# Kernel optimization log

Hardware: AMD Instinct MI355X
Metric: run time of the kernel (lower is better)

The kernel has to match this reference:

```python
import jax, jax.numpy as jnp
import numpy as np

B, S, D_IN, D_MODEL, H = 2, 2048, 1024, 1024, 16
DEPTH = D_MODEL // H


def setup_inputs() -> dict:
    key = jax.random.key(0)
    ks = jax.random.split(key, 12)
    f32 = jnp.float32
    scale = 0.02  # typical init scale for linear weights
    inp = {
        "v": jax.random.normal(ks[0], (B, S, D_IN), f32),
        "k": jax.random.normal(ks[1], (B, S, D_IN), f32),
        "q": jax.random.normal(ks[2], (B, S, D_IN), f32),
        # padding mask: 1 -> masked out, 0 -> keep; broadcastable to (B,H,Sq,Sk)
        "mask": jax.random.randint(ks[3], (B, 1, 1, S), 0, 2).astype(f32),
        # linear params stored as [in, out] so y = x @ W + b (matches torch Linear math)
        "Wq": jax.random.normal(ks[4], (D_IN, D_MODEL), f32) * scale,
        "bq": jnp.zeros((D_MODEL,), f32),
        "Wk": jax.random.normal(ks[5], (D_IN, D_MODEL), f32) * scale,
        "bk": jnp.zeros((D_MODEL,), f32),
        "Wv": jax.random.normal(ks[6], (D_IN, D_MODEL), f32) * scale,
        "bv": jnp.zeros((D_MODEL,), f32),
        "Wo": jax.random.normal(ks[7], (D_MODEL, D_MODEL), f32) * scale,
        "bo": jnp.zeros((D_MODEL,), f32),
    }
    return inp


def _split_heads(x):
    # [B, S, D_MODEL] -> [B, H, S, DEPTH]
    b = x.shape[0]
    return x.reshape(b, -1, H, DEPTH).transpose(0, 2, 1, 3)


def reference(v, k, q, mask, Wq, bq, Wk, bk, Wv, bv, Wo, bo):
    qh = _split_heads(q @ Wq + bq)   # [B,H,Sq,D]
    kh = _split_heads(k @ Wk + bk)   # [B,H,Sk,D]
    vh = _split_heads(v @ Wv + bv)   # [B,H,Sk,D]

    # scaled dot-product attention with additive mask (mask * -1e9)
    inv_sqrt_dk = 1.0 / jnp.sqrt(jnp.float32(DEPTH))
    logits = jnp.einsum('bhqd,bhkd->bhqk', qh, kh) * inv_sqrt_dk
    logits = logits + mask * (-1e9)
    attn = jax.nn.softmax(logits, axis=-1)          # [B,H,Sq,Sk]
    ctx = jnp.einsum('bhqk,bhkd->bhqd', attn, vh)   # [B,H,Sq,D]

    b = q.shape[0]
    concat = ctx.transpose(0, 2, 1, 3).reshape(b, -1, D_MODEL)  # [B,Sq,D_MODEL]
    out = concat @ Wo + bo
    return out, attn
```

## Files before the change

kernel.cpp:

```cpp
#include <hip/hip_runtime.h>
#include <cstdint>
#include <cstddef>

typedef __attribute__((ext_vector_type(4))) float f4;
typedef __attribute__((ext_vector_type(8))) short bf16x8;
typedef __attribute__((ext_vector_type(8))) unsigned short u16x8;
typedef unsigned long long u64;

__device__ __forceinline__ unsigned short f2bf(float x) {
    unsigned u = __float_as_uint(x);
    u += 0x7fffu + ((u >> 16) & 1u);
    return (unsigned short)(u >> 16);
}
__device__ __forceinline__ float bf2f(unsigned short h) {
    return __uint_as_float(((unsigned)h) << 16);
}
__device__ __forceinline__ float fast_exp2(float x) { return __builtin_amdgcn_exp2f(x); }
__device__ __forceinline__ float fast_log2(float x) { return __builtin_amdgcn_logf(x); }
__device__ __forceinline__ void gll16(const void* g, void* l) {
    __builtin_amdgcn_global_load_lds(
        (const __attribute__((address_space(1))) unsigned int*)g,
        (__attribute__((address_space(3))) unsigned int*)l, 16, 0, 0);
}
__device__ __forceinline__ f4 mfma16(bf16x8 a, bf16x8 b, f4 c) {
    return __builtin_amdgcn_mfma_f32_16x16x32_bf16(a, b, c, 0, 0, 0);
}

__global__ __launch_bounds__(256)
void prep_w_kernel(const float* __restrict__ Wq, const float* __restrict__ Wk,
                   const float* __restrict__ Wv, const float* __restrict__ Wo,
                   unsigned short* __restrict__ wt)
{
    const int w = blockIdx.z;
    const float* W = w == 0 ? Wq : (w == 1 ? Wk : (w == 2 ? Wv : Wo));
    unsigned short* hi = wt + (size_t)w * 1048576;

    const int kb = blockIdx.x << 6, nb = blockIdx.y << 6;
    __shared__ float T[64][68];
    const int tid = threadIdx.x;
    {
        const int r = tid >> 2, c0 = (tid & 3) << 4;
        const float* src = W + (size_t)(kb + r) * 1024 + nb + c0;
        *(f4*)&T[r][c0 + 0]  = *(const f4*)(src + 0);
        *(f4*)&T[r][c0 + 4]  = *(const f4*)(src + 4);
        *(f4*)&T[r][c0 + 8]  = *(const f4*)(src + 8);
        *(f4*)&T[r][c0 + 12] = *(const f4*)(src + 12);
    }
    __syncthreads();
    {
        const int n = tid & 63, ks = (tid >> 6) << 4;
        unsigned short vh[16];
        #pragma unroll
        for (int j = 0; j < 16; ++j) vh[j] = f2bf(T[ks + j][n]);
        const size_t dst = (size_t)(nb + n) * 1024 + kb + ks;
        *(u16x8*)(hi + dst)     = *(u16x8*)&vh[0];
        *(u16x8*)(hi + dst + 8) = *(u16x8*)&vh[8];
    }
}

__global__ __launch_bounds__(256)
void prep_a_kernel(const float* __restrict__ q, const float* __restrict__ k,
                   const float* __restrict__ v, unsigned short* __restrict__ a_hi)
{
    const int gid = blockIdx.x * 256 + threadIdx.x;
    const int z = gid >> 18;
    const int rem = gid & 262143;
    const float* src = z == 0 ? q : (z == 1 ? k : v);
    const size_t off = (size_t)rem << 4;
    const float* s = src + off;
    unsigned short* hi = a_hi + ((size_t)z << 22) + off;
    float xs[16];
    *(f4*)&xs[0]  = *(const f4*)(s + 0);
    *(f4*)&xs[4]  = *(const f4*)(s + 4);
    *(f4*)&xs[8]  = *(const f4*)(s + 8);
    *(f4*)&xs[12] = *(const f4*)(s + 12);
    unsigned short hv[16];
    #pragma unroll
    for (int j = 0; j < 16; ++j) hv[j] = f2bf(xs[j]);
    *(u16x8*)(hi + 0) = *(u16x8*)&hv[0];
    *(u16x8*)(hi + 8) = *(u16x8*)&hv[8];
}

__device__ __forceinline__ void gemm1_core(
    const unsigned short* __restrict__ AH, const unsigned short* __restrict__ WH,
    const float* __restrict__ bias, int bm, int bn, int mode,
    unsigned short* __restrict__ o_hi, float* __restrict__ o_f32, unsigned char* lds)
{
    unsigned char* As = lds;
    unsigned char* Bs = lds + 16384;

    const int tid = threadIdx.x, lane = tid & 63, wave = tid >> 6;
    const int wm = wave >> 1, wn = wave & 1;
    const int cx = lane & 15, lg = lane >> 4;
    const int l3 = lane >> 3, p3 = lane & 7;
    const int m0 = bm << 7, n0 = bn << 7;

    f4 acc[4][4];
    #pragma unroll
    for (int i = 0; i < 4; ++i)
        #pragma unroll
        for (int j = 0; j < 4; ++j) acc[i][j] = (f4){0.f, 0.f, 0.f, 0.f};

    #pragma unroll 1
    for (int k0 = 0; k0 < 1024; k0 += 64) {
        __syncthreads();
        #pragma unroll
        for (int c = 0; c < 4; ++c) {
            const int cb = (c << 2) + wave;
            const int row = (cb << 3) + l3;
            const int lgx = p3 ^ (row & 7);
            gll16(AH + (size_t)(m0 + row) * 1024 + k0 + (lgx << 3),
                  As + (cb << 10) + (lane << 4));
            gll16(WH + (size_t)(n0 + row) * 1024 + k0 + (lgx << 3),
                  Bs + (cb << 10) + (lane << 4));
        }
        __syncthreads();
        #pragma unroll
        for (int ks = 0; ks < 2; ++ks) {
            bf16x8 ah[4], bh[4];
            #pragma unroll
            for (int t = 0; t < 4; ++t) {
                const int r = (wm << 6) + (t << 4) + cx;
                ah[t] = *(const bf16x8*)(As + r * 128 + (((((ks << 2) + lg)) ^ (r & 7)) << 4));
                const int n = (wn << 6) + (t << 4) + cx;
                bh[t] = *(const bf16x8*)(Bs + n * 128 + (((((ks << 2) + lg)) ^ (n & 7)) << 4));
            }
            #pragma unroll
            for (int i = 0; i < 4; ++i)
                #pragma unroll
                for (int j = 0; j < 4; ++j)
                    acc[i][j] = mfma16(ah[i], bh[j], acc[i][j]);
        }
    }

    float bv4[4];
    #pragma unroll
    for (int j = 0; j < 4; ++j) bv4[j] = bias[n0 + (wn << 6) + (j << 4) + cx];

    #pragma unroll
    for (int i = 0; i < 4; ++i)
        #pragma unroll
        for (int j = 0; j < 4; ++j) {
            const int n = n0 + (wn << 6) + (j << 4) + cx;
            const int mb = m0 + (wm << 6) + (i << 4) + (lg << 2);
            if (mode == 2) {
                #pragma unroll
                for (int r = 0; r < 4; ++r)
                    o_f32[(size_t)(mb + r) * 1024 + n] = acc[i][j][r] + bv4[j];
            } else if (mode == 1) {
                const int b = mb >> 11, hh = n >> 6, d = n & 63;
                #pragma unroll
                for (int r = 0; r < 4; ++r) {
                    const int s = (mb + r) & 2047;
                    o_hi[(((size_t)(b * 16 + hh)) * 2048 + s) * 64 + d] = f2bf(acc[i][j][r] + bv4[j]);
                }
            } else {
                const int b = mb >> 11, s = mb & 2047;
                const int hh = n >> 6, d = n & 63;
                const unsigned short p0 = f2bf(acc[i][j][0] + bv4[j]);
                const unsigned short p1 = f2bf(acc[i][j][1] + bv4[j]);
                const unsigned short p2 = f2bf(acc[i][j][2] + bv4[j]);
                const unsigned short p3v = f2bf(acc[i][j][3] + bv4[j]);
                const u64 pk = (u64)p0 | ((u64)p1 << 16) | ((u64)p2 << 32) | ((u64)p3v << 48);
                *(u64*)&o_hi[((((size_t)(b * 16 + hh)) * 64 + d) << 11) + s] = pk;
            }
        }
}

__global__ __launch_bounds__(256)
void qkv_gemm_kernel(const unsigned short* __restrict__ a_hi,
                     const unsigned short* __restrict__ wt,
                     const float* __restrict__ bq, const float* __restrict__ bk,
                     const float* __restrict__ bv,
                     unsigned short* __restrict__ q_hi, unsigned short* __restrict__ k_hi,
                     unsigned short* __restrict__ vT)
{
    __shared__ __align__(16) unsigned char lds[32768];
    const int f = blockIdx.x;
    const int id2 = (f & 7) * 96 + (f >> 3);
    const int z = id2 >> 8;
    const int rem = id2 & 255;
    const int bn = rem >> 5, bm = rem & 31;
    const unsigned short* AH = a_hi + ((size_t)z << 22);
    const unsigned short* WH = wt + (size_t)z * 1048576;
    const float* bias = z == 0 ? bq : (z == 1 ? bk : bv);
    unsigned short* ohi = z == 0 ? q_hi : (z == 1 ? k_hi : vT);
    gemm1_core(AH, WH, bias, bm, bn, (z == 2) ? 3 : 1, ohi, nullptr, lds);
}

__global__ __launch_bounds__(256)
void out_gemm_kernel(const unsigned short* __restrict__ ctx_hi,
                     const unsigned short* __restrict__ wt_o,
                     const float* __restrict__ bo, float* __restrict__ out)
{
    __shared__ __align__(16) unsigned char lds[32768];
    const int f = blockIdx.x;
    const int id2 = (f & 7) * 32 + (f >> 3);
    const int bn = id2 >> 5, bm = id2 & 31;
    gemm1_core(ctx_hi, wt_o, bo, bm, bn, 2, nullptr, out, lds);
}

__global__ __launch_bounds__(256, 4)
void attn_kernel(const unsigned short* __restrict__ q_hi, const unsigned short* __restrict__ k_hi,
                 const unsigned short* __restrict__ vT, const float* __restrict__ mask,
                 float* __restrict__ attn, unsigned short* __restrict__ ctx_hi)
{
    __shared__ __align__(16) unsigned char lds[40960];
    unsigned char* K1 = lds;
    unsigned char* Vs = lds + 16384;
    unsigned char* Ps = lds + 32768;

    const int f = blockIdx.x;
    const int swzf = (f & 7) * 128 + (f >> 3);
    const int bh = swzf >> 5;
    const int q0 = (swzf & 31) << 6;
    const int b = bh >> 4, h = bh & 15;
    const int tid = threadIdx.x, lane = tid & 63, wave = tid >> 6;
    const int cx = lane & 15, lg = lane >> 4;
    const int l3 = lane >> 3, p3 = lane & 7;
    const size_t base = (size_t)bh * 131072;
    const float* mg = mask + (size_t)b * 2048;

    constexpr float C2   = 0.18033688011112042f;
    constexpr float M2   = -1.4426950408889634e9f;
    constexpr float MFIX = 4.0f;

    #pragma unroll
    for (int c = 0; c < 2; ++c) {
        const int cb = (c << 2) + wave;
        const int row = (cb << 3) + l3;
        const int lgx = p3 ^ (row & 7);
        gll16(q_hi + base + (size_t)(q0 + row) * 64 + (lgx << 3),
              Ps + (cb << 10) + (lane << 4));
        gll16(k_hi + base + (size_t)row * 64 + (lgx << 3),
              K1 + (cb << 10) + (lane << 4));
    }
    f4 mrc[4];
    #pragma unroll
    for (int nt = 0; nt < 4; ++nt) mrc[nt] = *(const f4*)(mg + (nt << 4) + (lg << 2));
    asm volatile("s_waitcnt vmcnt(0)" ::: "memory");
    __builtin_amdgcn_s_barrier();

    bf16x8 qb[2];
    {
        const int r = (wave << 4) + cx;
        const int mk = r & 7;
        #pragma unroll
        for (int ks = 0; ks < 2; ++ks)
            qb[ks] = *(const bf16x8*)(Ps + r * 128 + (((((ks << 2) + lg)) ^ mk) << 4));
    }

    float l_loc = 0.f;
    #pragma unroll 1
    for (int t = 0; t < 32; ++t) {
        const int p = t & 1;
        const int k0 = t << 6;
        f4 mrn[4];
        if (t < 31) {
            #pragma unroll
            for (int c = 0; c < 2; ++c) {
                const int cb = (c << 2) + wave;
                const int row = (cb << 3) + l3;
                const int lgx = p3 ^ (row & 7);
                gll16(k_hi + base + (size_t)(k0 + 64 + row) * 64 + (lgx << 3),
                      K1 + ((p ^ 1) << 13) + (cb << 10) + (lane << 4));
            }
            #pragma unroll
            for (int nt = 0; nt < 4; ++nt)
                mrn[nt] = *(const f4*)(mg + k0 + 64 + (nt << 4) + (lg << 2));
        }
        const unsigned char* Kc = K1 + (p << 13);
        #pragma unroll
        for (int nt = 0; nt < 4; ++nt) {
            const int kr = (nt << 4) + cx;
            const int mk = kr & 7;
            f4 s = (f4){0.f, 0.f, 0.f, 0.f};
            #pragma unroll
            for (int ks = 0; ks < 2; ++ks) {
                const bf16x8 kb = *(const bf16x8*)(Kc + kr * 128 + (((((ks << 2) + lg)) ^ mk) << 4));
                s = mfma16(kb, qb[ks], s);
            }
            #pragma unroll
            for (int r = 0; r < 4; ++r)
                l_loc += fast_exp2(fmaf(s[r], C2, fmaf(mrc[nt][r], M2, -MFIX)));
        }
        #pragma unroll
        for (int nt = 0; nt < 4; ++nt) mrc[nt] = mrn[nt];
        asm volatile("s_waitcnt vmcnt(4)" ::: "memory");
        __builtin_amdgcn_s_barrier();
    }
    float ssum = l_loc;
    ssum += __shfl_xor(ssum, 16);
    ssum += __shfl_xor(ssum, 32);
    const float cofs = -MFIX - fast_log2(ssum);

    #pragma unroll
    for (int c = 0; c < 2; ++c) {
        const int cb = (c << 2) + wave;
        const int row = (cb << 3) + l3;
        const int lgx = p3 ^ (row & 7);
        gll16(k_hi + base + (size_t)row * 64 + (lgx << 3),
              K1 + (cb << 10) + (lane << 4));
        gll16(vT + base + ((size_t)row << 11) + (lgx << 3),
              Vs + (cb << 10) + (lane << 4));
    }
    #pragma unroll
    for (int nt = 0; nt < 4; ++nt) mrc[nt] = *(const f4*)(mg + (nt << 4) + (lg << 2));
    asm volatile("s_waitcnt vmcnt(0)" ::: "memory");
    __builtin_amdgcn_s_barrier();

    f4 cacc[4];
    #pragma unroll
    for (int nt = 0; nt < 4; ++nt) cacc[nt] = (f4){0.f, 0.f, 0.f, 0.f};

    float* arow = attn + ((size_t)bh * 2048 + q0 + (wave << 4) + cx) * 2048;
    const unsigned psSwz = (unsigned)((cx & 7) << 4);

    #pragma unroll 1
    for (int t = 0; t < 32; ++t) {
        const int p = t & 1;
        const int k0 = t << 6;
        f4 mrn[4];
        if (t < 31) {
            #pragma unroll
            for (int c = 0; c < 2; ++c) {
                const int cb = (c << 2) + wave;
                const int row = (cb << 3) + l3;
                const int lgx = p3 ^ (row & 7);
                gll16(k_hi + base + (size_t)(k0 + 64 + row) * 64 + (lgx << 3),
                      K1 + ((p ^ 1) << 13) + (cb << 10) + (lane << 4));
                gll16(vT + base + ((size_t)row << 11) + k0 + 64 + (lgx << 3),
                      Vs + ((p ^ 1) << 13) + (cb << 10) + (lane << 4));
            }
            #pragma unroll
            for (int nt = 0; nt < 4; ++nt)
                mrn[nt] = *(const f4*)(mg + k0 + 64 + (nt << 4) + (lg << 2));
        }
        const unsigned char* Kc = K1 + (p << 13);
        f4 s[4];
        #pragma unroll
        for (int nt = 0; nt < 4; ++nt) {
            const int kr = (nt << 4) + cx;
            const int mk = kr & 7;
            s[nt] = (f4){0.f, 0.f, 0.f, 0.f};
            #pragma unroll
            for (int ks = 0; ks < 2; ++ks) {
                const bf16x8 kb = *(const bf16x8*)(Kc + kr * 128 + (((((ks << 2) + lg)) ^ mk) << 4));
                s[nt] = mfma16(kb, qb[ks], s[nt]);
            }
        }
        #pragma unroll
        for (int nt = 0; nt < 4; ++nt) {
            f4 pv;
            #pragma unroll
            for (int r = 0; r < 4; ++r)
                pv[r] = fast_exp2(fmaf(s[nt][r], C2, fmaf(mrc[nt][r], M2, cofs)));
            *(f4*)(arow + k0 + (nt << 4) + (lg << 2)) = pv;
            const unsigned w0 = (unsigned)f2bf(pv[0]) | ((unsigned)f2bf(pv[1]) << 16);
            const unsigned w1 = (unsigned)f2bf(pv[2]) | ((unsigned)f2bf(pv[3]) << 16);
            const u64 packed = (u64)w0 | ((u64)w1 << 32);
            *(u64*)(Ps + (((wave << 4) + cx) * 128) +
                    ((unsigned)((nt << 5) + (lg << 3)) ^ psSwz)) = packed;
        }
        #pragma unroll
        for (int nt = 0; nt < 4; ++nt) mrc[nt] = mrn[nt];
        #pragma unroll
        for (int ks = 0; ks < 2; ++ks) {
            const bf16x8 pa = *(const bf16x8*)(Ps + (((wave << 4) + cx) * 128) +
                                ((unsigned)((ks << 6) + (lg << 4)) ^ psSwz));
            #pragma unroll
            for (int nt = 0; nt < 4; ++nt) {
                const int dr = (nt << 4) + cx;
                const bf16x8 vb = *(const bf16x8*)(Vs + (p << 13) + dr * 128 +
                                    (((((ks << 2) + lg)) ^ (dr & 7)) << 4));
                cacc[nt] = mfma16(pa, vb, cacc[nt]);
            }
        }
        asm volatile("s_waitcnt vmcnt(8)" ::: "memory");
        __builtin_amdgcn_s_barrier();
    }

    #pragma unroll
    for (int nt = 0; nt < 4; ++nt)
        #pragma unroll
        for (int r = 0; r < 4; ++r) {
            const int srow = q0 + (wave << 4) + (lg << 2) + r;
            const int d = (h << 6) + (nt << 4) + cx;
            ctx_hi[((size_t)b * 2048 + srow) * 1024 + d] = f2bf(cacc[nt][r]);
        }
}

extern "C" void kernel_launch(void* const* d_in, const int* in_sizes, int n_in,
                              void* d_out, int out_size, void* d_ws, size_t ws_size,
                              hipStream_t stream)
{
    const float* v_in = (const float*)d_in[0];
    const float* k_in = (const float*)d_in[1];
    const float* q_in = (const float*)d_in[2];
    const float* mask = (const float*)d_in[3];
    const float* Wq = (const float*)d_in[4];
    const float* bq = (const float*)d_in[5];
    const float* Wk = (const float*)d_in[6];
    const float* bk = (const float*)d_in[7];
    const float* Wv = (const float*)d_in[8];
    const float* bv = (const float*)d_in[9];
    const float* Wo = (const float*)d_in[10];
    const float* bo = (const float*)d_in[11];

    float* out  = (float*)d_out;
    float* attn = out + (size_t)4194304;

    unsigned char* ws = (unsigned char*)d_ws;
    unsigned short* wt     = (unsigned short*)(ws);
    unsigned short* q_hi   = (unsigned short*)(ws + (size_t)(8)  * 1048576);
    unsigned short* k_hi   = (unsigned short*)(ws + (size_t)(16) * 1048576);
    unsigned short* vT     = (unsigned short*)(ws + (size_t)(24) * 1048576);
    unsigned short* ctx_hi = (unsigned short*)(ws + (size_t)(32) * 1048576);

    unsigned short* a_hi   = (unsigned short*)(attn + (size_t)60 * 1048576);

    prep_w_kernel<<<dim3(16, 16, 4), 256, 0, stream>>>(Wq, Wk, Wv, Wo, wt);
    prep_a_kernel<<<3072, 256, 0, stream>>>(q_in, k_in, v_in, a_hi);
    qkv_gemm_kernel<<<768, 256, 0, stream>>>(a_hi, wt, bq, bk, bv, q_hi, k_hi, vT);
    attn_kernel<<<1024, 256, 0, stream>>>(q_hi, k_hi, vT, mask, attn, ctx_hi);
    out_gemm_kernel<<<256, 256, 0, stream>>>(ctx_hi, wt + (size_t)3 * 1048576, bo, out);
}
```

Measured before the change: 308.3 us.

## Add separate V transpose kernel, set MFMA priority, retune attention waitcnts

The QKV GEMM now writes V in head-major [B,H,S,D] layout like Q and K, and a new LDS-based transpose kernel produces the transposed V used by attention. This replaces the scattered 8-byte transposed stores in the GEMM epilogue. The attention kernel wraps its MFMA sections in s_setprio to favour matrix issue, splits score computation from the exp accumulation, and changes the vmcnt wait thresholds, making the first pass wait on all loads. The cost is an extra kernel launch, an extra round trip of V through memory, and possibly less load overlap from the stricter waits.

```diff
diff --git a/kernel.cpp b/kernel.cpp
--- a/kernel.cpp
+++ b/kernel.cpp
@@ -81,6 +81,34 @@
     *(u16x8*)(hi + 8) = *(u16x8*)&hv[8];
 }
 
+__global__ __launch_bounds__(256)
+void vtr_kernel(const unsigned short* __restrict__ v_hi, unsigned short* __restrict__ vT)
+{
+    __shared__ unsigned short T[64][80];
+    const int bh = blockIdx.y;
+    const int s0 = blockIdx.x << 6;
+    const int tid = threadIdx.x;
+    const size_t base = (size_t)bh * 131072;
+    {
+        const int s = tid >> 2, dq = (tid & 3) << 4;
+        const unsigned short* src = v_hi + base + (size_t)(s0 + s) * 64 + dq;
+        u16x8 a = *(const u16x8*)src;
+        u16x8 b = *(const u16x8*)(src + 8);
+        *(u16x8*)&T[s][dq]     = a;
+        *(u16x8*)&T[s][dq + 8] = b;
+    }
+    __syncthreads();
+    {
+        const int d = tid >> 2, sq = (tid & 3) << 4;
+        unsigned short o[16];
+        #pragma unroll
+        for (int j = 0; j < 16; ++j) o[j] = T[sq + j][d];
+        unsigned short* dst = vT + base + ((size_t)d << 11) + s0 + sq;
+        *(u16x8*)dst       = *(u16x8*)&o[0];
+        *(u16x8*)(dst + 8) = *(u16x8*)&o[8];
+    }
+}
+
 __device__ __forceinline__ void gemm1_core(
     const unsigned short* __restrict__ AH, const unsigned short* __restrict__ WH,
     const float* __restrict__ bias, int bm, int bn, int mode,
@@ -147,22 +175,13 @@
                 #pragma unroll
                 for (int r = 0; r < 4; ++r)
                     o_f32[(size_t)(mb + r) * 1024 + n] = acc[i][j][r] + bv4[j];
-            } else if (mode == 1) {
+            } else {
                 const int b = mb >> 11, hh = n >> 6, d = n & 63;
                 #pragma unroll
                 for (int r = 0; r < 4; ++r) {
                     const int s = (mb + r) & 2047;
                     o_hi[(((size_t)(b * 16 + hh)) * 2048 + s) * 64 + d] = f2bf(acc[i][j][r] + bv4[j]);
                 }
-            } else {
-                const int b = mb >> 11, s = mb & 2047;
-                const int hh = n >> 6, d = n & 63;
-                const unsigned short p0 = f2bf(acc[i][j][0] + bv4[j]);
-                const unsigned short p1 = f2bf(acc[i][j][1] + bv4[j]);
-                const unsigned short p2 = f2bf(acc[i][j][2] + bv4[j]);
-                const unsigned short p3v = f2bf(acc[i][j][3] + bv4[j]);
-                const u64 pk = (u64)p0 | ((u64)p1 << 16) | ((u64)p2 << 32) | ((u64)p3v << 48);
-                *(u64*)&o_hi[((((size_t)(b * 16 + hh)) * 64 + d) << 11) + s] = pk;
             }
         }
 }
@@ -173,7 +192,7 @@
                      const float* __restrict__ bq, const float* __restrict__ bk,
                      const float* __restrict__ bv,
                      unsigned short* __restrict__ q_hi, unsigned short* __restrict__ k_hi,
-                     unsigned short* __restrict__ vT)
+                     unsigned short* __restrict__ v_hi)
 {
     __shared__ __align__(16) unsigned char lds[32768];
     const int f = blockIdx.x;
@@ -184,8 +203,8 @@
     const unsigned short* AH = a_hi + ((size_t)z << 22);
     const unsigned short* WH = wt + (size_t)z * 1048576;
     const float* bias = z == 0 ? bq : (z == 1 ? bk : bv);
-    unsigned short* ohi = z == 0 ? q_hi : (z == 1 ? k_hi : vT);
-    gemm1_core(AH, WH, bias, bm, bn, (z == 2) ? 3 : 1, ohi, nullptr, lds);
+    unsigned short* ohi = z == 0 ? q_hi : (z == 1 ? k_hi : v_hi);
+    gemm1_core(AH, WH, bias, bm, bn, 1, ohi, nullptr, lds);
 }
 
 __global__ __launch_bounds__(256)
@@ -270,6 +289,8 @@
                 mrn[nt] = *(const f4*)(mg + k0 + 64 + (nt << 4) + (lg << 2));
         }
         const unsigned char* Kc = K1 + (p << 13);
+        __builtin_amdgcn_s_setprio(1);
+        f4 sv[4];
         #pragma unroll
         for (int nt = 0; nt < 4; ++nt) {
             const int kr = (nt << 4) + cx;
@@ -280,13 +301,17 @@
                 const bf16x8 kb = *(const bf16x8*)(Kc + kr * 128 + (((((ks << 2) + lg)) ^ mk) << 4));
                 s = mfma16(kb, qb[ks], s);
             }
+            sv[nt] = s;
+        }
+        __builtin_amdgcn_s_setprio(0);
+        #pragma unroll
+        for (int nt = 0; nt < 4; ++nt)
             #pragma unroll
             for (int r = 0; r < 4; ++r)
-                l_loc += fast_exp2(fmaf(s[r], C2, fmaf(mrc[nt][r], M2, -MFIX)));
-        }
+                l_loc += fast_exp2(fmaf(sv[nt][r], C2, fmaf(mrc[nt][r], M2, -MFIX)));
         #pragma unroll
         for (int nt = 0; nt < 4; ++nt) mrc[nt] = mrn[nt];
-        asm volatile("s_waitcnt vmcnt(4)" ::: "memory");
+        asm volatile("s_waitcnt vmcnt(0)" ::: "memory");
         __builtin_amdgcn_s_barrier();
     }
     float ssum = l_loc;
@@ -338,6 +363,7 @@
         }
         const unsigned char* Kc = K1 + (p << 13);
         f4 s[4];
+        __builtin_amdgcn_s_setprio(1);
         #pragma unroll
         for (int nt = 0; nt < 4; ++nt) {
             const int kr = (nt << 4) + cx;
@@ -349,6 +375,7 @@
                 s[nt] = mfma16(kb, qb[ks], s[nt]);
             }
         }
+        __builtin_amdgcn_s_setprio(0);
         #pragma unroll
         for (int nt = 0; nt < 4; ++nt) {
             f4 pv;
@@ -364,6 +391,7 @@
         }
         #pragma unroll
         for (int nt = 0; nt < 4; ++nt) mrc[nt] = mrn[nt];
+        __builtin_amdgcn_s_setprio(1);
         #pragma unroll
         for (int ks = 0; ks < 2; ++ks) {
             const bf16x8 pa = *(const bf16x8*)(Ps + (((wave << 4) + cx) * 128) +
@@ -376,7 +404,8 @@
                 cacc[nt] = mfma16(pa, vb, cacc[nt]);
             }
         }
-        asm volatile("s_waitcnt vmcnt(8)" ::: "memory");
+        __builtin_amdgcn_s_setprio(0);
+        asm volatile("s_waitcnt vmcnt(4)" ::: "memory");
         __builtin_amdgcn_s_barrier();
     }
 
@@ -414,14 +443,16 @@
     unsigned short* wt     = (unsigned short*)(ws);
     unsigned short* q_hi   = (unsigned short*)(ws + (size_t)(8)  * 1048576);
     unsigned short* k_hi   = (unsigned short*)(ws + (size_t)(16) * 1048576);
-    unsigned short* vT     = (unsigned short*)(ws + (size_t)(24) * 1048576);
+    unsigned short* v_hi   = (unsigned short*)(ws + (size_t)(24) * 1048576);
     unsigned short* ctx_hi = (unsigned short*)(ws + (size_t)(32) * 1048576);
+    unsigned short* vT     = (unsigned short*)(ws + (size_t)(40) * 1048576);
 
     unsigned short* a_hi   = (unsigned short*)(attn + (size_t)60 * 1048576);
 
     prep_w_kernel<<<dim3(16, 16, 4), 256, 0, stream>>>(Wq, Wk, Wv, Wo, wt);
     prep_a_kernel<<<3072, 256, 0, stream>>>(q_in, k_in, v_in, a_hi);
-    qkv_gemm_kernel<<<768, 256, 0, stream>>>(a_hi, wt, bq, bk, bv, q_hi, k_hi, vT);
+    qkv_gemm_kernel<<<768, 256, 0, stream>>>(a_hi, wt, bq, bk, bv, q_hi, k_hi, v_hi);
+    vtr_kernel<<<dim3(32, 32), 256, 0, stream>>>(v_hi, vT);
     attn_kernel<<<1024, 256, 0, stream>>>(q_hi, k_hi, vT, mask, attn, ctx_hi);
     out_gemm_kernel<<<256, 256, 0, stream>>>(ctx_hi, wt + (size_t)3 * 1048576, bo, out);
 }
```

After: 293.2 us. 4.9% less time.

## Transpose V through LDS, prioritise MFMA waves, and pack bf16 conversions

Applied to the files above, without the earlier changes.

Adds a GEMM epilogue (mode 3) that stages the V projection tile in swizzled LDS and writes V^T with 16-byte vector stores, replacing scattered 8-byte transposed stores. In the attention kernel it raises wave priority around the MFMA blocks and adds scheduling barriers after the prefetch issue. It also splits the row-sum accumulator into four independent chains and uses the hardware packed bf16 conversion instruction for P. The vmcnt wait in the second loop is tightened from 8 to 4, which may add stall time. The old mode-0 epilogue is folded into the mode-1 path, so correctness depends on the launcher now passing mode 3 for V.

```diff
diff --git a/kernel.cpp b/kernel.cpp
--- a/kernel.cpp
+++ b/kernel.cpp
@@ -14,6 +14,11 @@
 }
 __device__ __forceinline__ float bf2f(unsigned short h) {
     return __uint_as_float(((unsigned)h) << 16);
+}
+__device__ __forceinline__ unsigned cvtpk_bf16(float lo, float hi) {
+    unsigned r;
+    asm("v_cvt_pk_bf16_f32 %0, %1, %2" : "=v"(r) : "v"(lo), "v"(hi));
+    return r;
 }
 __device__ __forceinline__ float fast_exp2(float x) { return __builtin_amdgcn_exp2f(x); }
 __device__ __forceinline__ float fast_log2(float x) { return __builtin_amdgcn_logf(x); }
@@ -137,6 +142,35 @@
     #pragma unroll
     for (int j = 0; j < 4; ++j) bv4[j] = bias[n0 + (wn << 6) + (j << 4) + cx];
 
+    if (mode == 3) {
+        __syncthreads();
+        unsigned short* T = (unsigned short*)lds;
+        #pragma unroll
+        for (int i = 0; i < 4; ++i)
+            #pragma unroll
+            for (int j = 0; j < 4; ++j) {
+                const int dl = (wn << 6) + (j << 4) + cx;
+                #pragma unroll
+                for (int r = 0; r < 4; ++r) {
+                    const int sl = (wm << 6) + (i << 4) + (lg << 2) + r;
+                    T[sl * 128 + (dl ^ ((sl & 7) << 3))] = f2bf(acc[i][j][r] + bv4[j]);
+                }
+            }
+        __syncthreads();
+        const int b = m0 >> 11, s0g = m0 & 2047;
+        const int dl = tid >> 1, sc = (tid & 1) << 6;
+        const int hh = (n0 + dl) >> 6, d = (n0 + dl) & 63;
+        unsigned short ov[64];
+        #pragma unroll
+        for (int j = 0; j < 64; ++j)
+            ov[j] = T[(sc + j) * 128 + (dl ^ (((sc + j) & 7) << 3))];
+        unsigned short* dst = o_hi + ((((size_t)(b * 16 + hh)) * 64 + d) << 11) + s0g + sc;
+        #pragma unroll
+        for (int c8 = 0; c8 < 8; ++c8)
+            *(u16x8*)(dst + (c8 << 3)) = *(u16x8*)&ov[c8 << 3];
+        return;
+    }
+
     #pragma unroll
     for (int i = 0; i < 4; ++i)
         #pragma unroll
@@ -147,22 +181,13 @@
                 #pragma unroll
                 for (int r = 0; r < 4; ++r)
                     o_f32[(size_t)(mb + r) * 1024 + n] = acc[i][j][r] + bv4[j];
-            } else if (mode == 1) {
+            } else {
                 const int b = mb >> 11, hh = n >> 6, d = n & 63;
                 #pragma unroll
                 for (int r = 0; r < 4; ++r) {
                     const int s = (mb + r) & 2047;
                     o_hi[(((size_t)(b * 16 + hh)) * 2048 + s) * 64 + d] = f2bf(acc[i][j][r] + bv4[j]);
                 }
-            } else {
-                const int b = mb >> 11, s = mb & 2047;
-                const int hh = n >> 6, d = n & 63;
-                const unsigned short p0 = f2bf(acc[i][j][0] + bv4[j]);
-                const unsigned short p1 = f2bf(acc[i][j][1] + bv4[j]);
-                const unsigned short p2 = f2bf(acc[i][j][2] + bv4[j]);
-                const unsigned short p3v = f2bf(acc[i][j][3] + bv4[j]);
-                const u64 pk = (u64)p0 | ((u64)p1 << 16) | ((u64)p2 << 32) | ((u64)p3v << 48);
-                *(u64*)&o_hi[((((size_t)(b * 16 + hh)) * 64 + d) << 11) + s] = pk;
             }
         }
 }
@@ -250,7 +275,7 @@
             qb[ks] = *(const bf16x8*)(Ps + r * 128 + (((((ks << 2) + lg)) ^ mk) << 4));
     }
 
-    float l_loc = 0.f;
+    float l4[4] = {0.f, 0.f, 0.f, 0.f};
     #pragma unroll 1
     for (int t = 0; t < 32; ++t) {
         const int p = t & 1;
@@ -265,11 +290,14 @@
                 gll16(k_hi + base + (size_t)(k0 + 64 + row) * 64 + (lgx << 3),
                       K1 + ((p ^ 1) << 13) + (cb << 10) + (lane << 4));
             }
+            __builtin_amdgcn_sched_barrier(0);
             #pragma unroll
             for (int nt = 0; nt < 4; ++nt)
                 mrn[nt] = *(const f4*)(mg + k0 + 64 + (nt << 4) + (lg << 2));
         }
         const unsigned char* Kc = K1 + (p << 13);
+        __builtin_amdgcn_s_setprio(1);
+        f4 sv[4];
         #pragma unroll
         for (int nt = 0; nt < 4; ++nt) {
             const int kr = (nt << 4) + cx;
@@ -280,16 +308,20 @@
                 const bf16x8 kb = *(const bf16x8*)(Kc + kr * 128 + (((((ks << 2) + lg)) ^ mk) << 4));
                 s = mfma16(kb, qb[ks], s);
             }
+            sv[nt] = s;
+        }
+        __builtin_amdgcn_s_setprio(0);
+        #pragma unroll
+        for (int nt = 0; nt < 4; ++nt)
             #pragma unroll
             for (int r = 0; r < 4; ++r)
-                l_loc += fast_exp2(fmaf(s[r], C2, fmaf(mrc[nt][r], M2, -MFIX)));
-        }
+                l4[nt] += fast_exp2(fmaf(sv[nt][r], C2, fmaf(mrc[nt][r], M2, -MFIX)));
         #pragma unroll
         for (int nt = 0; nt < 4; ++nt) mrc[nt] = mrn[nt];
         asm volatile("s_waitcnt vmcnt(4)" ::: "memory");
         __builtin_amdgcn_s_barrier();
     }
-    float ssum = l_loc;
+    float ssum = (l4[0] + l4[1]) + (l4[2] + l4[3]);
     ssum += __shfl_xor(ssum, 16);
     ssum += __shfl_xor(ssum, 32);
     const float cofs = -MFIX - fast_log2(ssum);
@@ -332,12 +364,14 @@
                 gll16(vT + base + ((size_t)row << 11) + k0 + 64 + (lgx << 3),
                       Vs + ((p ^ 1) << 13) + (cb << 10) + (lane << 4));
             }
+            __builtin_amdgcn_sched_barrier(0);
             #pragma unroll
             for (int nt = 0; nt < 4; ++nt)
                 mrn[nt] = *(const f4*)(mg + k0 + 64 + (nt << 4) + (lg << 2));
         }
         const unsigned char* Kc = K1 + (p << 13);
         f4 s[4];
+        __builtin_amdgcn_s_setprio(1);
         #pragma unroll
         for (int nt = 0; nt < 4; ++nt) {
             const int kr = (nt << 4) + cx;
@@ -349,6 +383,7 @@
                 s[nt] = mfma16(kb, qb[ks], s[nt]);
             }
         }
+        __builtin_amdgcn_s_setprio(0);
         #pragma unroll
         for (int nt = 0; nt < 4; ++nt) {
             f4 pv;
@@ -356,14 +391,15 @@
             for (int r = 0; r < 4; ++r)
                 pv[r] = fast_exp2(fmaf(s[nt][r], C2, fmaf(mrc[nt][r], M2, cofs)));
             *(f4*)(arow + k0 + (nt << 4) + (lg << 2)) = pv;
-            const unsigned w0 = (unsigned)f2bf(pv[0]) | ((unsigned)f2bf(pv[1]) << 16);
-            const unsigned w1 = (unsigned)f2bf(pv[2]) | ((unsigned)f2bf(pv[3]) << 16);
+            const unsigned w0 = cvtpk_bf16(pv[0], pv[1]);
+            const unsigned w1 = cvtpk_bf16(pv[2], pv[3]);
             const u64 packed = (u64)w0 | ((u64)w1 << 32);
             *(u64*)(Ps + (((wave << 4) + cx) * 128) +
                     ((unsigned)((nt << 5) + (lg << 3)) ^ psSwz)) = packed;
         }
         #pragma unroll
         for (int nt = 0; nt < 4; ++nt) mrc[nt] = mrn[nt];
+        __builtin_amdgcn_s_setprio(1);
         #pragma unroll
         for (int ks = 0; ks < 2; ++ks) {
             const bf16x8 pa = *(const bf16x8*)(Ps + (((wave << 4) + cx) * 128) +
@@ -376,7 +412,8 @@
                 cacc[nt] = mfma16(pa, vb, cacc[nt]);
             }
         }
-        asm volatile("s_waitcnt vmcnt(8)" ::: "memory");
+        __builtin_amdgcn_s_setprio(0);
+        asm volatile("s_waitcnt vmcnt(4)" ::: "memory");
         __builtin_amdgcn_s_barrier();
     }
 
```

Result: faster. 292.7 us (-5.1%).
